# Performance work log

Measured on AMD Instinct MI355X. Metric: run time of the kernel, lower is better.

## Reference

```python
import jax, jax.numpy as jnp
import numpy as np

N = 8192
H_CHANNELS = 2048
HEADS = 16
D = H_CHANNELS // HEADS  # 128


def setup_inputs() -> dict:
    key = jax.random.key(0)
    k1, k2, k3 = jax.random.split(key, 3)
    x0 = jax.random.normal(k1, (N, H_CHANNELS), dtype=jnp.float32)
    # boolean mask: True entries are masked out (set to -inf)
    mask = jax.random.randint(k2, (N, N), 0, 2).astype(jnp.bool_)
    # torch Linear weight layout: [out_features, in_features] = [3*d, h_channels]
    W_qkv = jax.random.normal(k3, (3 * D, H_CHANNELS), dtype=jnp.float32) * (1.0 / np.sqrt(H_CHANNELS))
    return {"x0": x0, "mask": mask, "W_qkv": W_qkv}


def reference(x0, mask, W_qkv):
    # qkv = x0 @ W^T : [N, 3d]
    qkv = x0 @ W_qkv.T
    q, k, v = jnp.split(qkv, 3, axis=-1)          # each [N, d]
    att_logits = (q @ k.T) / D                    # [N, N]  (note: scale is /d, not /sqrt(d))
    att_logits = jnp.where(mask, -jnp.inf, att_logits)
    att = jax.nn.softmax(att_logits, axis=-1)     # [N, N]
    # dropout p=0.0 (eval mode) -> identity
    return att @ v                                # [N, d]
```

## Files before the change

kernel.cpp:

```cpp
#include <hip/hip_runtime.h>
#include <hip/hip_bf16.h>

typedef __attribute__((ext_vector_type(8))) short short8;
typedef __attribute__((ext_vector_type(4))) float f32x4;

#define NTOK 8192
#define HCH  2048
#define DDIM 128
#define NSPLIT 8
#define KPS   (NTOK / NSPLIT)
#define NITER (KPS / 64)

__device__ __forceinline__ unsigned short f2bf(float f) {
    __hip_bfloat16 h = __float2bfloat16(f);
    return *reinterpret_cast<unsigned short*>(&h);
}
__device__ __forceinline__ unsigned short f2h(float f) {
    _Float16 h = (_Float16)f;
    return *reinterpret_cast<unsigned short*>(&h);
}

__device__ __forceinline__ void gload_lds16(const void* g, void* l) {
    __builtin_amdgcn_global_load_lds(
        reinterpret_cast<const __attribute__((address_space(1))) unsigned int*>(
            reinterpret_cast<uintptr_t>(g)),
        reinterpret_cast<__attribute__((address_space(3))) unsigned int*>(
            reinterpret_cast<uintptr_t>(l)),
        16, 0, 0);
}

__global__ void detect_kernel(const unsigned int* __restrict__ X,
                              const unsigned int* __restrict__ M,
                              int* __restrict__ flags)
{
    const int lane = threadIdx.x & 63;
    unsigned int e = (X[lane] >> 7) & 0xFF;
    unsigned long long hb = __ballot(e >= 110 && e <= 140);

    bool w_ok = true, h_ok = true, b_ok = true;
#pragma unroll
    for (int i = 0; i < 16; i++) {
        unsigned int u = M[lane + 64 * i];
        if (!(u == 0u || u == 1u || u == 0x3F800000u)) w_ok = false;
        unsigned int h0 = u & 0xFFFFu, h1 = u >> 16;
        bool o0 = (h0 == 0u || h0 == 0x3F80u || h0 == 0x3C00u || h0 == 1u);
        bool o1 = (h1 == 0u || h1 == 0x3F80u || h1 == 0x3C00u || h1 == 1u);
        if (!(o0 && o1)) h_ok = false;
        unsigned int b0 = u & 0xFF, b1 = (u >> 8) & 0xFF,
                     b2 = (u >> 16) & 0xFF, b3 = u >> 24;
        if (b0 > 1u || b1 > 1u || b2 > 1u || b3 > 1u) b_ok = false;
    }
    bool allw = __all(w_ok), allh = __all(h_ok), allb = __all(b_ok);
    if (lane == 0) {
        flags[0] = (__popcll(hb) < 32) ? 1 : 0;
        flags[1] = allw ? 0 : (allb ? 1 : (allh ? 2 : 3));
    }
}

__global__ __launch_bounds__(256) void conv_w(
    const void* __restrict__ Wv, const int* __restrict__ flags,
    unsigned short* __restrict__ Wbf)
{
    int t = blockIdx.x * 256 + threadIdx.x;
    size_t off = (size_t)t * 8;
    if (flags[0] != 0) {
        const float* Wf = (const float*)Wv;
        float4 a = *reinterpret_cast<const float4*>(Wf + off);
        float4 b = *reinterpret_cast<const float4*>(Wf + off + 4);
        unsigned short o[8] = { f2bf(a.x), f2bf(a.y), f2bf(a.z), f2bf(a.w),
                                f2bf(b.x), f2bf(b.y), f2bf(b.z), f2bf(b.w) };
        *reinterpret_cast<uint4*>(Wbf + off) = *reinterpret_cast<uint4*>(o);
    } else {
        *reinterpret_cast<uint4*>(Wbf + off) =
            *reinterpret_cast<const uint4*>((const unsigned short*)Wv + off);
    }
}

__global__ __launch_bounds__(256) void conv_x(
    const void* __restrict__ Xv, const int* __restrict__ flags,
    unsigned short* __restrict__ Xbf)
{
    int t = blockIdx.x * 256 + threadIdx.x;
    size_t off = (size_t)t * 8;
    if (flags[0] != 0) {
        const float* Xf = (const float*)Xv;
        float4 a = *reinterpret_cast<const float4*>(Xf + off);
        float4 b = *reinterpret_cast<const float4*>(Xf + off + 4);
        unsigned short o[8] = { f2bf(a.x), f2bf(a.y), f2bf(a.z), f2bf(a.w),
                                f2bf(b.x), f2bf(b.y), f2bf(b.z), f2bf(b.w) };
        *reinterpret_cast<uint4*>(Xbf + off) = *reinterpret_cast<uint4*>(o);
    } else {
        *reinterpret_cast<uint4*>(Xbf + off) =
            *reinterpret_cast<const uint4*>((const unsigned short*)Xv + off);
    }
}

__global__ __launch_bounds__(256) void mask_pack(
    const void* __restrict__ maskv, const int* __restrict__ flags,
    unsigned char* __restrict__ Mp)
{
    const int mmode = flags[1];
    const int NB = NTOK * (NTOK / 8);
    int t0 = blockIdx.x * 256 + threadIdx.x;
    for (int b = t0; b < NB; b += 2048 * 256) {
        unsigned int byte = 0;
        if (mmode == 0) {
            const uint4* p = reinterpret_cast<const uint4*>(
                (const unsigned int*)maskv + (size_t)b * 8);
            uint4 a = p[0], c = p[1];
            byte = (a.x != 0u) | ((a.y != 0u) << 1) | ((a.z != 0u) << 2) | ((a.w != 0u) << 3)
                 | ((c.x != 0u) << 4) | ((c.y != 0u) << 5) | ((c.z != 0u) << 6) | ((c.w != 0u) << 7);
        } else if (mmode == 1) {
            unsigned long long v = *reinterpret_cast<const unsigned long long*>(
                (const unsigned char*)maskv + (size_t)b * 8);
#pragma unroll
            for (int k = 0; k < 8; k++)
                byte |= (((v >> (8 * k)) & 0xFFull) != 0ull) << k;
        } else if (mmode == 2) {
            uint4 a = *reinterpret_cast<const uint4*>(
                (const unsigned short*)maskv + (size_t)b * 8);
            byte = ((a.x & 0xFFFFu) != 0u) | ((a.x >> 16 != 0u) << 1)
                 | (((a.y & 0xFFFFu) != 0u) << 2) | ((a.y >> 16 != 0u) << 3)
                 | (((a.z & 0xFFFFu) != 0u) << 4) | ((a.z >> 16 != 0u) << 5)
                 | (((a.w & 0xFFFFu) != 0u) << 6) | ((a.w >> 16 != 0u) << 7);
        } else {
            byte = ((const unsigned char*)maskv)[b];
        }
        Mp[b] = (unsigned char)byte;
    }
}

__global__ __launch_bounds__(256) void qkv_gemm(
    const unsigned short* __restrict__ Xbf, const unsigned short* __restrict__ Wbf,
    unsigned short* __restrict__ Qb, unsigned short* __restrict__ Kb,
    unsigned short* __restrict__ Vb)
{
    __shared__ unsigned short Wsm[128 * 64];
    __shared__ unsigned short Xsm[32 * 64];
    const int tid  = threadIdx.x;
    const int lane = tid & 63, w = tid >> 6;
    const int c = lane & 15, g = lane >> 4;
    const int q0 = blockIdx.x * 32;
    const int n0 = blockIdx.y * 128;

    f32x4 acc[4];
#pragma unroll
    for (int i = 0; i < 4; i++) acc[i] = (f32x4){0.f, 0.f, 0.f, 0.f};

    const int xrow = tid >> 3, xc8 = tid & 7;
    const int arow = (w & 1) * 16 + c;

    for (int kk = 0; kk < HCH; kk += 64) {
        __syncthreads();
#pragma unroll
        for (int i = 0; i < 4; i++) {
            int cid = tid + 256 * i;
            int n = cid >> 3, c8 = cid & 7;
            gload_lds16(Wbf + (size_t)(n0 + n) * HCH + kk + ((c8 ^ (n & 7)) * 8),
                        &Wsm[cid * 8]);
        }
        gload_lds16(Xbf + (size_t)(q0 + xrow) * HCH + kk + ((xc8 ^ (xrow & 7)) * 8),
                    &Xsm[tid * 8]);
        __syncthreads();
#pragma unroll
        for (int ks = 0; ks < 2; ks++) {
            short8 af = *reinterpret_cast<const short8*>(
                &Xsm[(arow * 8 + ((ks * 4 + g) ^ (c & 7))) * 8]);
#pragma unroll
            for (int nt = 0; nt < 4; nt++) {
                int n = (w >> 1) * 64 + nt * 16 + c;
                short8 bf = *reinterpret_cast<const short8*>(
                    &Wsm[(n * 8 + ((ks * 4 + g) ^ (c & 7))) * 8]);
                acc[nt] = __builtin_amdgcn_mfma_f32_16x16x32_bf16(af, bf, acc[nt], 0, 0, 0);
            }
        }
    }
    unsigned short* dst = (blockIdx.y == 0) ? Qb : (blockIdx.y == 1) ? Kb : Vb;
#pragma unroll
    for (int nt = 0; nt < 4; nt++) {
        int n = (w >> 1) * 64 + nt * 16 + c;
#pragma unroll
        for (int r = 0; r < 4; r++) {
            int rr = q0 + (w & 1) * 16 + g * 4 + r;
            dst[(size_t)rr * DDIM + n] = f2bf(acc[nt][r]);
        }
    }
}

__global__ __launch_bounds__(256) void vtrans(
    const unsigned short* __restrict__ V, unsigned short* __restrict__ VT)
{
    __shared__ unsigned short T[32 * 33];
    const int t = threadIdx.x;
    const int k0 = blockIdx.x * 32, d0 = blockIdx.y * 32;
    {
        int key = t >> 3, dq = (t & 7) * 4;
        ushort4 v = *reinterpret_cast<const ushort4*>(V + (size_t)(k0 + key) * DDIM + d0 + dq);
        T[(dq + 0) * 33 + key] = v.x;
        T[(dq + 1) * 33 + key] = v.y;
        T[(dq + 2) * 33 + key] = v.z;
        T[(dq + 3) * 33 + key] = v.w;
    }
    __syncthreads();
    {
        int d = t >> 3, kq = (t & 7) * 4;
        ushort4 o;
        o.x = T[d * 33 + kq + 0]; o.y = T[d * 33 + kq + 1];
        o.z = T[d * 33 + kq + 2]; o.w = T[d * 33 + kq + 3];
        *reinterpret_cast<ushort4*>(VT + (size_t)(d0 + d) * NTOK + k0 + kq) = o;
    }
}

__global__ __launch_bounds__(256) void attn_part(
    const unsigned short* __restrict__ Qb, const unsigned short* __restrict__ Kb,
    const unsigned short* __restrict__ VT, const unsigned long long* __restrict__ Mp,
    _Float16* __restrict__ Opart, float* __restrict__ lpart)
{
    __shared__ unsigned short Ksm[2][64 * 128];
    __shared__ unsigned short Vsm[2][128 * 64];
    __shared__ unsigned short Psm[4 * 16 * 64];
    const int tid  = threadIdx.x;
    const int lane = tid & 63, w = tid >> 6;
    const int c = lane & 15, g = lane >> 4;
    const int split = blockIdx.x;
    const int qb    = blockIdx.y;
    const int q0 = qb * 128;
    const int kbase = split * KPS;
    const int tb0 = kbase >> 6;
    unsigned short* Pw = &Psm[w * 16 * 64];

    auto stage = [&](int b, int tt) {
        const int k0s = kbase + tt * 64;
#pragma unroll
        for (int i = 0; i < 4; i++) {
            int cid = tid + 256 * i;
            int rowk = cid >> 4, c16 = cid & 15;
            gload_lds16(Kb + (size_t)(k0s + rowk) * DDIM + ((c16 ^ (rowk & 15)) * 8),
                        &Ksm[b][cid * 8]);
        }
#pragma unroll
        for (int i = 0; i < 4; i++) {
            int cid = tid + 256 * i;
            int d = cid >> 3, c8 = cid & 7;
            gload_lds16(VT + (size_t)d * NTOK + k0s + ((c8 ^ (d & 7)) * 8),
                        &Vsm[b][cid * 8]);
        }
    };

    short8 qf[2][4];
#pragma unroll
    for (int rt = 0; rt < 2; rt++)
#pragma unroll
        for (int ks = 0; ks < 4; ks++)
            qf[rt][ks] = *reinterpret_cast<const short8*>(
                Qb + (size_t)(q0 + w * 32 + rt * 16 + c) * DDIM + ks * 32 + g * 8);

    short8 ones;
#pragma unroll
    for (int i = 0; i < 8; i++) ones[i] = (short)0x3F80;

    f32x4 accO[2][8];
#pragma unroll
    for (int rt = 0; rt < 2; rt++)
#pragma unroll
        for (int i = 0; i < 8; i++) accO[rt][i] = (f32x4){0.f, 0.f, 0.f, 0.f};
    f32x4 accL[2] = {(f32x4){0.f,0.f,0.f,0.f}, (f32x4){0.f,0.f,0.f,0.f}};

    unsigned long long mp[2][4], mpn[2][4];
#pragma unroll
    for (int rt = 0; rt < 2; rt++)
#pragma unroll
        for (int r = 0; r < 4; r++)
            mp[rt][r] = Mp[(size_t)(q0 + w * 32 + rt * 16 + g * 4 + r) * 128 + tb0];

    stage(0, 0);

    for (int t = 0; t < NITER; t++) {
        __syncthreads();
        if (t + 1 < NITER) {
            stage((t + 1) & 1, t + 1);
#pragma unroll
            for (int rt = 0; rt < 2; rt++)
#pragma unroll
                for (int r = 0; r < 4; r++)
                    mpn[rt][r] = Mp[(size_t)(q0 + w * 32 + rt * 16 + g * 4 + r) * 128 + tb0 + t + 1];
        }
        const unsigned short* Ks = Ksm[t & 1];
        const unsigned short* Vs = Vsm[t & 1];

#pragma unroll
        for (int rt = 0; rt < 2; rt++) {
            f32x4 sacc[4];
#pragma unroll
            for (int nt = 0; nt < 4; nt++) {
                sacc[nt] = (f32x4){0.f, 0.f, 0.f, 0.f};
#pragma unroll
                for (int ks = 0; ks < 4; ks++) {
                    short8 bf = *reinterpret_cast<const short8*>(
                        &Ks[((nt * 16 + c) * 16 + ((ks * 4 + g) ^ c)) * 8]);
                    sacc[nt] = __builtin_amdgcn_mfma_f32_16x16x32_bf16(qf[rt][ks], bf, sacc[nt], 0, 0, 0);
                }
            }
#pragma unroll
            for (int nt = 0; nt < 4; nt++)
#pragma unroll
                for (int r = 0; r < 4; r++) {
                    bool mv = (mp[rt][r] >> (nt * 16 + c)) & 1ull;
                    float p = mv ? 0.f : __expf(sacc[nt][r] * (1.0f / 128.0f));
                    int row = g * 4 + r;
                    Pw[(row * 8 + ((nt * 2 + (c >> 3)) ^ (row & 7))) * 8 + (c & 7)] = f2bf(p);
                }
#pragma unroll
            for (int ks2 = 0; ks2 < 2; ks2++) {
                short8 af = *reinterpret_cast<const short8*>(
                    &Pw[(c * 8 + ((ks2 * 4 + g) ^ (c & 7))) * 8]);
                accL[rt] = __builtin_amdgcn_mfma_f32_16x16x32_bf16(af, ones, accL[rt], 0, 0, 0);
#pragma unroll
                for (int dt = 0; dt < 8; dt++) {
                    short8 bfv = *reinterpret_cast<const short8*>(
                        &Vs[((dt * 16 + c) * 8 + ((ks2 * 4 + g) ^ (c & 7))) * 8]);
                    accO[rt][dt] = __builtin_amdgcn_mfma_f32_16x16x32_bf16(af, bfv, accO[rt][dt], 0, 0, 0);
                }
            }
        }
#pragma unroll
        for (int rt = 0; rt < 2; rt++)
#pragma unroll
            for (int r = 0; r < 4; r++) mp[rt][r] = mpn[rt][r];
    }

    _Float16* Ob = Opart + ((size_t)split * 64 + qb) * (128 * DDIM) + (size_t)w * 4096;
#pragma unroll
    for (int rt = 0; rt < 2; rt++)
#pragma unroll
        for (int r = 0; r < 4; r++) {
            unsigned short o[8];
#pragma unroll
            for (int dt = 0; dt < 8; dt++) o[dt] = f2h(accO[rt][dt][r]);
            *reinterpret_cast<uint4*>(Ob + ((((rt * 4 + r) * 4 + g) * 16 + c) * 8)) =
                *reinterpret_cast<uint4*>(o);
        }
    if (c == 0) {
#pragma unroll
        for (int rt = 0; rt < 2; rt++)
#pragma unroll
            for (int r = 0; r < 4; r++)
                lpart[(size_t)split * NTOK + q0 + w * 32 + rt * 16 + g * 4 + r] = accL[rt][r];
    }
}

__global__ __launch_bounds__(256) void combine(
    const _Float16* __restrict__ Opart, const float* __restrict__ lpart,
    float* __restrict__ out)
{
    int cid = blockIdx.x * 256 + threadIdx.x;
    int c = cid & 15, g = (cid >> 4) & 3, r = (cid >> 6) & 3;
    int rt = (cid >> 8) & 1, w = (cid >> 9) & 3, qb = cid >> 11;
    int row = qb * 128 + w * 32 + rt * 16 + g * 4 + r;
    size_t base = (size_t)qb * (128 * DDIM) + (size_t)w * 4096
                + ((((rt * 4 + r) * 4 + g) * 16 + c) * 8);
    const size_t S = (size_t)NTOK * DDIM;
    float den = 0.f;
    float num[8] = {0.f, 0.f, 0.f, 0.f, 0.f, 0.f, 0.f, 0.f};
#pragma unroll
    for (int s = 0; s < NSPLIT; s++) {
        den += lpart[(size_t)s * NTOK + row];
        uint4 v = *reinterpret_cast<const uint4*>(Opart + (size_t)s * S + base);
        const _Float16* h = reinterpret_cast<const _Float16*>(&v);
#pragma unroll
        for (int dt = 0; dt < 8; dt++) num[dt] += (float)h[dt];
    }
    float inv = (den > 0.f) ? (1.f / den) : 0.f;
#pragma unroll
    for (int dt = 0; dt < 8; dt++)
        out[(size_t)row * DDIM + dt * 16 + c] = num[dt] * inv;
}

extern "C" void kernel_launch(void* const* d_in, const int* in_sizes, int n_in,
                              void* d_out, int out_size, void* d_ws, size_t ws_size,
                              hipStream_t stream)
{
    const void* X = d_in[0]; const void* mask = d_in[1]; const void* W = d_in[2];
    {
        const void* x_ = nullptr; const void* m_ = nullptr; const void* w_ = nullptr;
        for (int i = 0; i < n_in; i++) {
            if (in_sizes[i] == 16777216) x_ = d_in[i];
            else if (in_sizes[i] == 67108864) m_ = d_in[i];
            else if (in_sizes[i] == 786432) w_ = d_in[i];
        }
        if (x_ && m_ && w_) { X = x_; mask = m_; W = w_; }
    }
    float* out = (float*)d_out;

    char* ws = (char*)d_ws;
    unsigned short* Qb  = (unsigned short*)(ws);
    unsigned short* Kb  = (unsigned short*)(ws + (2ull << 20));
    unsigned short* VT  = (unsigned short*)(ws + (4ull << 20));
    unsigned long long* Mpk = (unsigned long long*)(ws + (6ull << 20));
    _Float16*       Opart = (_Float16*)(ws + (14ull << 20));
    unsigned short* Wbf = (unsigned short*)(ws + (14ull << 20));
    unsigned short* Vb  = (unsigned short*)(ws + (14ull << 20) + (1536ull << 10));
    float*          lpart = (float*)(ws + (30ull << 20));
    int*            flags = (int*)(ws + (30ull << 20) + (512ull << 10));
    unsigned short* Xbf = (unsigned short*)(ws + (32ull << 20));

    detect_kernel<<<1, 64, 0, stream>>>((const unsigned int*)X, (const unsigned int*)mask, flags);
    conv_w<<<dim3(384), 256, 0, stream>>>(W, flags, Wbf);
    conv_x<<<dim3(8192), 256, 0, stream>>>(X, flags, Xbf);
    mask_pack<<<dim3(2048), 256, 0, stream>>>(mask, flags, (unsigned char*)Mpk);
    qkv_gemm<<<dim3(256, 3), 256, 0, stream>>>(Xbf, Wbf, Qb, Kb, Vb);
    vtrans<<<dim3(256, 4), 256, 0, stream>>>(Vb, VT);
    attn_part<<<dim3(NSPLIT, 64), 256, 0, stream>>>(Qb, Kb, VT, Mpk, Opart, lpart);
    combine<<<dim3(4096 / 8), 256, 0, stream>>>(Opart, lpart, out);
}
```

Before: 535.5 us.

## Rewrite attention core with 32x32 MFMA and register-resident P via permlane swap

Switches the attention partial kernel from 16x16x32 to 32x32x16 bf16 MFMA, computing S transposed (K as A operand) so each lane owns one query row. Probabilities are packed to bf16 with v_cvt_pk_bf16_f32 and rearranged with permlane32_swap directly into the A-operand layout for the PV product, removing the LDS round trip for P and the ones-MFMA used for row sums. Row sums are accumulated in scalar registers and combined with a cross-half shuffle. The output partial layout and combine kernel are reworked to match, with more combine blocks each handling fewer elements.

```diff
diff --git a/kernel.cpp b/kernel.cpp
--- a/kernel.cpp
+++ b/kernel.cpp
@@ -3,6 +3,8 @@
 
 typedef __attribute__((ext_vector_type(8))) short short8;
 typedef __attribute__((ext_vector_type(4))) float f32x4;
+typedef __attribute__((ext_vector_type(16))) float f32x16;
+typedef __attribute__((ext_vector_type(2))) unsigned int uint2v;
 
 #define NTOK 8192
 #define HCH  2048
@@ -218,16 +220,15 @@
 {
     __shared__ unsigned short Ksm[2][64 * 128];
     __shared__ unsigned short Vsm[2][128 * 64];
-    __shared__ unsigned short Psm[4 * 16 * 64];
     const int tid  = threadIdx.x;
     const int lane = tid & 63, w = tid >> 6;
-    const int c = lane & 15, g = lane >> 4;
+    const int la = lane & 31, hi = lane >> 5;
     const int split = blockIdx.x;
     const int qb    = blockIdx.y;
     const int q0 = qb * 128;
     const int kbase = split * KPS;
     const int tb0 = kbase >> 6;
-    unsigned short* Pw = &Psm[w * 16 * 64];
+    const int qrow = q0 + w * 32 + la;
 
     auto stage = [&](int b, int tt) {
         const int k0s = kbase + tt * 64;
@@ -247,31 +248,20 @@
         }
     };
 
-    short8 qf[2][4];
-#pragma unroll
-    for (int rt = 0; rt < 2; rt++)
-#pragma unroll
-        for (int ks = 0; ks < 4; ks++)
-            qf[rt][ks] = *reinterpret_cast<const short8*>(
-                Qb + (size_t)(q0 + w * 32 + rt * 16 + c) * DDIM + ks * 32 + g * 8);
-
-    short8 ones;
-#pragma unroll
-    for (int i = 0; i < 8; i++) ones[i] = (short)0x3F80;
-
-    f32x4 accO[2][8];
-#pragma unroll
-    for (int rt = 0; rt < 2; rt++)
-#pragma unroll
-        for (int i = 0; i < 8; i++) accO[rt][i] = (f32x4){0.f, 0.f, 0.f, 0.f};
-    f32x4 accL[2] = {(f32x4){0.f,0.f,0.f,0.f}, (f32x4){0.f,0.f,0.f,0.f}};
-
-    unsigned long long mp[2][4], mpn[2][4];
-#pragma unroll
-    for (int rt = 0; rt < 2; rt++)
-#pragma unroll
-        for (int r = 0; r < 4; r++)
-            mp[rt][r] = Mp[(size_t)(q0 + w * 32 + rt * 16 + g * 4 + r) * 128 + tb0];
+    short8 qf[8];
+#pragma unroll
+    for (int dstep = 0; dstep < 8; dstep++)
+        qf[dstep] = *reinterpret_cast<const short8*>(
+            Qb + (size_t)qrow * DDIM + dstep * 16 + hi * 8);
+
+    f32x16 accO[4];
+#pragma unroll
+    for (int dt = 0; dt < 4; dt++)
+#pragma unroll
+        for (int r = 0; r < 16; r++) accO[dt][r] = 0.f;
+    float Lacc = 0.f;
+
+    unsigned long long mw = Mp[(size_t)qrow * 128 + tb0], mwn = 0;
 
     stage(0, 0);
 
@@ -279,74 +269,83 @@
         __syncthreads();
         if (t + 1 < NITER) {
             stage((t + 1) & 1, t + 1);
-#pragma unroll
-            for (int rt = 0; rt < 2; rt++)
-#pragma unroll
-                for (int r = 0; r < 4; r++)
-                    mpn[rt][r] = Mp[(size_t)(q0 + w * 32 + rt * 16 + g * 4 + r) * 128 + tb0 + t + 1];
+            mwn = Mp[(size_t)qrow * 128 + tb0 + t + 1];
         }
         const unsigned short* Ks = Ksm[t & 1];
         const unsigned short* Vs = Vsm[t & 1];
 
-#pragma unroll
-        for (int rt = 0; rt < 2; rt++) {
-            f32x4 sacc[4];
-#pragma unroll
-            for (int nt = 0; nt < 4; nt++) {
-                sacc[nt] = (f32x4){0.f, 0.f, 0.f, 0.f};
-#pragma unroll
-                for (int ks = 0; ks < 4; ks++) {
-                    short8 bf = *reinterpret_cast<const short8*>(
-                        &Ks[((nt * 16 + c) * 16 + ((ks * 4 + g) ^ c)) * 8]);
-                    sacc[nt] = __builtin_amdgcn_mfma_f32_16x16x32_bf16(qf[rt][ks], bf, sacc[nt], 0, 0, 0);
-                }
+        f32x16 S0, S1;
+#pragma unroll
+        for (int r = 0; r < 16; r++) { S0[r] = 0.f; S1[r] = 0.f; }
+#pragma unroll
+        for (int dstep = 0; dstep < 8; dstep++) {
+            int slot = (2 * dstep + hi) ^ (la & 15);
+            short8 k0f = *reinterpret_cast<const short8*>(&Ks[(la * 16 + slot) * 8]);
+            short8 k1f = *reinterpret_cast<const short8*>(&Ks[((32 + la) * 16 + slot) * 8]);
+            S0 = __builtin_amdgcn_mfma_f32_32x32x16_bf16(k0f, qf[dstep], S0, 0, 0, 0);
+            S1 = __builtin_amdgcn_mfma_f32_32x32x16_bf16(k1f, qf[dstep], S1, 0, 0, 0);
+        }
+
+        const unsigned long long mh = mw >> (4 * hi);
+        short8 pa[4];
+        auto softpack = [&](const f32x16& S, int kt, short8* paP) {
+            float p[16];
+#pragma unroll
+            for (int r = 0; r < 16; r++) {
+                int bit = kt * 32 + (r & 3) + 8 * (r >> 2);
+                bool mv = (mh >> bit) & 1ull;
+                float e = __expf(S[r] * 0.0078125f);
+                p[r] = mv ? 0.f : e;
+                Lacc += p[r];
             }
-#pragma unroll
-            for (int nt = 0; nt < 4; nt++)
-#pragma unroll
-                for (int r = 0; r < 4; r++) {
-                    bool mv = (mp[rt][r] >> (nt * 16 + c)) & 1ull;
-                    float p = mv ? 0.f : __expf(sacc[nt][r] * (1.0f / 128.0f));
-                    int row = g * 4 + r;
-                    Pw[(row * 8 + ((nt * 2 + (c >> 3)) ^ (row & 7))) * 8 + (c & 7)] = f2bf(p);
-                }
-#pragma unroll
-            for (int ks2 = 0; ks2 < 2; ks2++) {
-                short8 af = *reinterpret_cast<const short8*>(
-                    &Pw[(c * 8 + ((ks2 * 4 + g) ^ (c & 7))) * 8]);
-                accL[rt] = __builtin_amdgcn_mfma_f32_16x16x32_bf16(af, ones, accL[rt], 0, 0, 0);
-#pragma unroll
-                for (int dt = 0; dt < 8; dt++) {
-                    short8 bfv = *reinterpret_cast<const short8*>(
-                        &Vs[((dt * 16 + c) * 8 + ((ks2 * 4 + g) ^ (c & 7))) * 8]);
-                    accO[rt][dt] = __builtin_amdgcn_mfma_f32_16x16x32_bf16(af, bfv, accO[rt][dt], 0, 0, 0);
-                }
+            unsigned int U[4][2];
+#pragma unroll
+            for (int b = 0; b < 4; b++) {
+                asm("v_cvt_pk_bf16_f32 %0, %1, %2"
+                    : "=v"(U[b][0]) : "v"(p[4 * b + 0]), "v"(p[4 * b + 1]));
+                asm("v_cvt_pk_bf16_f32 %0, %1, %2"
+                    : "=v"(U[b][1]) : "v"(p[4 * b + 2]), "v"(p[4 * b + 3]));
             }
-        }
-#pragma unroll
-        for (int rt = 0; rt < 2; rt++)
-#pragma unroll
-            for (int r = 0; r < 4; r++) mp[rt][r] = mpn[rt][r];
-    }
+#pragma unroll
+            for (int h = 0; h < 2; h++) {
+                uint2v sA = __builtin_amdgcn_permlane32_swap(U[2 * h][0], U[2 * h + 1][0], false, false);
+                uint2v sB = __builtin_amdgcn_permlane32_swap(U[2 * h][1], U[2 * h + 1][1], false, false);
+                unsigned int fr[4] = { sA.x, sB.x, sA.y, sB.y };
+                paP[h] = *reinterpret_cast<short8*>(fr);
+            }
+        };
+        softpack(S0, 0, &pa[0]);
+        softpack(S1, 1, &pa[2]);
+
+#pragma unroll
+        for (int s = 0; s < 4; s++) {
+#pragma unroll
+            for (int dt = 0; dt < 4; dt++) {
+                int slot = (2 * s + hi) ^ (la & 7);
+                short8 vf = *reinterpret_cast<const short8*>(
+                    &Vs[((dt * 32 + la) * 8 + slot) * 8]);
+                accO[dt] = __builtin_amdgcn_mfma_f32_32x32x16_bf16(pa[s], vf, accO[dt], 0, 0, 0);
+            }
+        }
+        if (t + 1 < NITER) mw = mwn;
+    }
+
+    Lacc += __shfl_xor(Lacc, 32, 64);
 
     _Float16* Ob = Opart + ((size_t)split * 64 + qb) * (128 * DDIM) + (size_t)w * 4096;
 #pragma unroll
-    for (int rt = 0; rt < 2; rt++)
-#pragma unroll
-        for (int r = 0; r < 4; r++) {
-            unsigned short o[8];
-#pragma unroll
-            for (int dt = 0; dt < 8; dt++) o[dt] = f2h(accO[rt][dt][r]);
-            *reinterpret_cast<uint4*>(Ob + ((((rt * 4 + r) * 4 + g) * 16 + c) * 8)) =
-                *reinterpret_cast<uint4*>(o);
-        }
-    if (c == 0) {
-#pragma unroll
-        for (int rt = 0; rt < 2; rt++)
-#pragma unroll
-            for (int r = 0; r < 4; r++)
-                lpart[(size_t)split * NTOK + q0 + w * 32 + rt * 16 + g * 4 + r] = accL[rt][r];
-    }
+    for (int dt = 0; dt < 4; dt++)
+#pragma unroll
+        for (int b = 0; b < 4; b++) {
+            unsigned int w0 = (unsigned int)f2h(accO[dt][4 * b + 0])
+                            | ((unsigned int)f2h(accO[dt][4 * b + 1]) << 16);
+            unsigned int w1 = (unsigned int)f2h(accO[dt][4 * b + 2])
+                            | ((unsigned int)f2h(accO[dt][4 * b + 3]) << 16);
+            uint2 uv; uv.x = w0; uv.y = w1;
+            *reinterpret_cast<uint2*>(Ob + (size_t)((dt * 4 + b) * 64 + lane) * 4) = uv;
+        }
+    if (hi == 0)
+        lpart[(size_t)split * NTOK + q0 + w * 32 + la] = Lacc;
 }
 
 __global__ __launch_bounds__(256) void combine(
@@ -354,26 +353,31 @@
     float* __restrict__ out)
 {
     int cid = blockIdx.x * 256 + threadIdx.x;
-    int c = cid & 15, g = (cid >> 4) & 3, r = (cid >> 6) & 3;
-    int rt = (cid >> 8) & 1, w = (cid >> 9) & 3, qb = cid >> 11;
-    int row = qb * 128 + w * 32 + rt * 16 + g * 4 + r;
-    size_t base = (size_t)qb * (128 * DDIM) + (size_t)w * 4096
-                + ((((rt * 4 + r) * 4 + g) * 16 + c) * 8);
+    int l  = cid & 63;
+    int b  = (cid >> 6) & 3;
+    int dt = (cid >> 8) & 3;
+    int w  = (cid >> 10) & 3;
+    int qb = cid >> 12;
+    int la = l & 31, hi = l >> 5;
+    int d  = dt * 32 + la;
+    int rbase = qb * 128 + w * 32 + 8 * b + 4 * hi;
+    size_t off = (size_t)qb * (128 * DDIM) + (size_t)w * 4096
+               + (size_t)((dt * 4 + b) * 64 + l) * 4;
     const size_t S = (size_t)NTOK * DDIM;
-    float den = 0.f;
-    float num[8] = {0.f, 0.f, 0.f, 0.f, 0.f, 0.f, 0.f, 0.f};
+    float num[4] = {0.f, 0.f, 0.f, 0.f};
+    float den[4] = {0.f, 0.f, 0.f, 0.f};
 #pragma unroll
     for (int s = 0; s < NSPLIT; s++) {
-        den += lpart[(size_t)s * NTOK + row];
-        uint4 v = *reinterpret_cast<const uint4*>(Opart + (size_t)s * S + base);
+        uint2 v = *reinterpret_cast<const uint2*>(Opart + (size_t)s * S + off);
         const _Float16* h = reinterpret_cast<const _Float16*>(&v);
 #pragma unroll
-        for (int dt = 0; dt < 8; dt++) num[dt] += (float)h[dt];
-    }
-    float inv = (den > 0.f) ? (1.f / den) : 0.f;
-#pragma unroll
-    for (int dt = 0; dt < 8; dt++)
-        out[(size_t)row * DDIM + dt * 16 + c] = num[dt] * inv;
+        for (int j = 0; j < 4; j++) num[j] += (float)h[j];
+#pragma unroll
+        for (int j = 0; j < 4; j++) den[j] += lpart[(size_t)s * NTOK + rbase + j];
+    }
+#pragma unroll
+    for (int j = 0; j < 4; j++)
+        out[(size_t)(rbase + j) * DDIM + d] = (den[j] > 0.f) ? num[j] / den[j] : 0.f;
 }
 
 extern "C" void kernel_launch(void* const* d_in, const int* in_sizes, int n_in,
@@ -411,5 +415,5 @@
     qkv_gemm<<<dim3(256, 3), 256, 0, stream>>>(Xbf, Wbf, Qb, Kb, Vb);
     vtrans<<<dim3(256, 4), 256, 0, stream>>>(Vb, VT);
     attn_part<<<dim3(NSPLIT, 64), 256, 0, stream>>>(Qb, Kb, VT, Mpk, Opart, lpart);
-    combine<<<dim3(4096 / 8), 256, 0, stream>>>(Opart, lpart, out);
-}
+    combine<<<dim3(1024), 256, 0, stream>>>(Opart, lpart, out);
+}
```

Measured after the change: 525.1 us. No clear change (-1.9%).
